# Kernel optimization log

Hardware: AMD Instinct MI355X
Metric: run time of the kernel (lower is better)

The kernel has to match this reference:

```python
import jax, jax.numpy as jnp
import numpy as np


def _lstm_last(x, wih, whh, bih, bhh):
    """PyTorch-semantics LSTM over x [B, T, I]; returns last hidden state [B, H].
    Gate order in weights: i, f, g, o (PyTorch convention)."""
    B = x.shape[0]
    H = whh.shape[1]
    b = bih + bhh

    def step(carry, xt):
        h, c = carry
        g = xt @ wih.T + h @ whh.T + b  # [B, 4H]
        i, f, gg, o = jnp.split(g, 4, axis=-1)
        c = jax.nn.sigmoid(f) * c + jax.nn.sigmoid(i) * jnp.tanh(gg)
        h = jax.nn.sigmoid(o) * jnp.tanh(c)
        return (h, c), None

    h0 = jnp.zeros((B, H), x.dtype)
    (h, _), _ = jax.lax.scan(step, (h0, h0), jnp.swapaxes(x, 0, 1))
    return h


def setup_inputs() -> dict:
    key = jax.random.key(0)
    ks = jax.random.split(key, 16)
    B, N, T = 512, 32, 50
    s = 0.05
    return {
        "agent_traj": jax.random.normal(ks[0], (B, T, 2), jnp.float32),
        "neighbour_traj": jax.random.normal(ks[1], (B, N, T, 2), jnp.float32),
        "a_wih": jax.random.normal(ks[2], (256, 2), jnp.float32) * s,
        "a_whh": jax.random.normal(ks[3], (256, 64), jnp.float32) * s,
        "a_bih": jax.random.normal(ks[4], (256,), jnp.float32) * s,
        "a_bhh": jax.random.normal(ks[5], (256,), jnp.float32) * s,
        "n_wih": jax.random.normal(ks[6], (256, 2), jnp.float32) * s,
        "n_whh": jax.random.normal(ks[7], (256, 64), jnp.float32) * s,
        "n_bih": jax.random.normal(ks[8], (256,), jnp.float32) * s,
        "n_bhh": jax.random.normal(ks[9], (256,), jnp.float32) * s,
        "d_wih": jax.random.normal(ks[10], (512, 128), jnp.float32) * s,
        "d_whh": jax.random.normal(ks[11], (512, 128), jnp.float32) * s,
        "d_bih": jax.random.normal(ks[12], (512,), jnp.float32) * s,
        "d_bhh": jax.random.normal(ks[13], (512,), jnp.float32) * s,
        "e_w": jax.random.normal(ks[14], (2, 128), jnp.float32) * s,
        "e_b": jax.random.normal(ks[15], (2,), jnp.float32) * s,
    }


def reference(agent_traj, neighbour_traj, a_wih, a_whh, a_bih, a_bhh,
              n_wih, n_whh, n_bih, n_bhh, d_wih, d_whh, d_bih, d_bhh, e_w, e_b):
    B, N, T, _ = neighbour_traj.shape
    # agent encoder: last hidden state [B, 64]
    agent_emb = _lstm_last(agent_traj, a_wih, a_whh, a_bih, a_bhh)
    # neighbour encoder: batch all B*N ragged sequences as one LSTM call, then mean over neighbours
    nh = _lstm_last(neighbour_traj.reshape(B * N, T, 2), n_wih, n_whh, n_bih, n_bhh)
    neigh_emb = nh.reshape(B, N, 64).mean(axis=1)  # [B, 64]

    h0 = jnp.concatenate([agent_emb, neigh_emb], axis=1)  # [B, 128]
    c0 = jnp.zeros_like(h0)
    db = d_bih + d_bhh

    def dec_step(carry, _):
        h, c = carry
        # LSTMCell with input = h itself
        g = h @ d_wih.T + h @ d_whh.T + db  # [B, 512]
        i, f, gg, o = jnp.split(g, 4, axis=-1)
        c = jax.nn.sigmoid(f) * c + jax.nn.sigmoid(i) * jnp.tanh(gg)
        h = jax.nn.sigmoid(o) * jnp.tanh(c)
        pred = h @ e_w.T + e_b  # [B, 2]
        return (h, c), pred

    _, preds = jax.lax.scan(dec_step, (h0, c0), None, length=30)  # [30, B, 2]
    return jnp.swapaxes(preds, 0, 1)  # [B, 30, 2]
```

## Files before the change

kernel.cpp:

```cpp
#include <hip/hip_runtime.h>
#include <hip/hip_bf16.h>


typedef __attribute__((ext_vector_type(8))) short bf16x8;
typedef __attribute__((ext_vector_type(4))) float f32x4;
typedef unsigned int uint;
typedef unsigned short ushort_t;

#define LOG2E  1.4426950408889634f
#define LOG2E2 2.8853900817779268f

__device__ __forceinline__ float rcp_fast(float x) { return __builtin_amdgcn_rcpf(x); }
__device__ __forceinline__ float exp2_fast(float x) { return __builtin_amdgcn_exp2f(x); }
__device__ __forceinline__ float sigf(float x) { return rcp_fast(1.0f + __expf(-x)); }
__device__ __forceinline__ float tanh_fast(float x) {
    x = fminf(fmaxf(x, -15.0f), 15.0f);
    float e = __expf(2.0f * x);
    return (e - 1.0f) * rcp_fast(e + 1.0f);
}
__device__ __forceinline__ ushort_t bf_hi(float f) {
    union { float f; uint u; } v; v.f = f;
    return (ushort_t)(v.u >> 16);
}
__device__ __forceinline__ ushort_t bf_rtn(float f) {
    union { float f; uint u; } v; v.f = f;
    return (ushort_t)((v.u + 0x7FFFu + ((v.u >> 16) & 1u)) >> 16);
}
__device__ __forceinline__ float bf_f(ushort_t h) {
    union { float f; uint u; } v; v.u = ((uint)h) << 16;
    return v.f;
}

__device__ __forceinline__ float cell_update_p(float xi, float xf, float xg,
                                               float xo, float& c) {
    float pi = exp2_fast(-xi);
    float pf = exp2_fast(-xf);
    float po = exp2_fast(-xo);
    float pg = exp2_fast(fminf(xg, 120.0f));
    float A = 1.0f + pf;
    float B = 1.0f + pi;
    float C = 1.0f + pg;
    float BC = B * C;
    float R  = rcp_fast(A * BC);
    float num = __builtin_fmaf(c, BC, (C - 2.0f) * A);
    float cc = num * R;
    c = cc;
    float e2 = exp2_fast(fminf(cc * LOG2E2, 120.0f));
    return (e2 - 1.0f) * rcp_fast((1.0f + po) * (e2 + 1.0f));
}

#define HS 36

__global__ __launch_bounds__(256, 4) void enc14_kernel(
    const float* __restrict__ ax, const float* __restrict__ nx,
    const float* __restrict__ a_wih, const float* __restrict__ a_whh,
    const float* __restrict__ a_bih, const float* __restrict__ a_bhh,
    const float* __restrict__ n_wih, const float* __restrict__ n_whh,
    const float* __restrict__ n_bih, const float* __restrict__ n_bhh,
    float* __restrict__ nh_out, float* __restrict__ ah_out)
{
    const int tid = threadIdx.x, blk = blockIdx.x;
    const bool agent = (blk >= 1024);
    const int seq0 = (agent ? (blk - 1024) : blk) * 16;
    const float* __restrict__ x   = agent ? ax : nx;
    const float* __restrict__ wih = agent ? a_wih : n_wih;
    const float* __restrict__ whh = agent ? a_whh : n_whh;
    const float* __restrict__ bih = agent ? a_bih : n_bih;
    const float* __restrict__ bhh = agent ? a_bhh : n_bhh;
    float* __restrict__ hout = agent ? ah_out : nh_out;

    const int lane = tid & 63, wv = tid >> 6;
    const int col = lane & 15, quad = lane >> 4;

    __shared__ __attribute__((aligned(16))) uint hb[2][16][HS];
    __shared__ __attribute__((aligned(16))) ushort_t xb[50][16][8];

    bf16x8 Aw[4][2];
    #pragma unroll
    for (int g = 0; g < 4; ++g) {
        const float sc = (g == 2) ? LOG2E2 : LOG2E;
        #pragma unroll
        for (int kt = 0; kt < 2; ++kt) {
            const float* p = whh + (size_t)(g * 64 + 16 * wv + col) * 64 + kt * 32 + quad * 8;
            float4 v0 = *(const float4*)p;
            float4 v1 = *(const float4*)(p + 4);
            float vv[8] = { v0.x, v0.y, v0.z, v0.w, v1.x, v1.y, v1.z, v1.w };
            bf16x8 h8;
            #pragma unroll
            for (int j = 0; j < 8; ++j) h8[j] = (short)bf_rtn(vv[j] * sc);
            Aw[g][kt] = h8;
        }
    }

    bf16x8 Ax[4];
    #pragma unroll
    for (int g = 0; g < 4; ++g) {
        const float sc = (g == 2) ? LOG2E2 : LOG2E;
        bf16x8 a;
        #pragma unroll
        for (int j = 0; j < 8; ++j) a[j] = 0;
        if (quad == 0) {
            const int row = g * 64 + 16 * wv + col;
            float w0 = wih[2 * row] * sc, w1 = wih[2 * row + 1] * sc;
            float b  = (bih[row] + bhh[row]) * sc;
            ushort_t w0h = bf_hi(w0), w1h = bf_hi(w1);
            ushort_t bh  = bf_hi(b);
            a[0] = (short)w0h;
            a[1] = (short)w1h;
            a[2] = (short)bf_hi(w0 - bf_f(w0h));
            a[3] = (short)bf_hi(w1 - bf_f(w1h));
            a[4] = (short)w0h;
            a[5] = (short)w1h;
            a[6] = (short)bh;
            a[7] = (short)bf_hi(b - bf_f(bh));
        }
        Ax[g] = a;
    }

    for (int idx = tid; idx < 50 * 16; idx += 256) {
        const int t = idx >> 4, s = idx & 15;
        const float* xp = x + (size_t)(seq0 + s) * 100 + 2 * t;
        float x0 = xp[0], x1 = xp[1];
        ushort_t h0 = bf_hi(x0), h1 = bf_hi(x1);
        ushort_t* e = &xb[t][s][0];
        e[0] = h0; e[1] = h1;
        e[2] = h0; e[3] = h1;
        e[4] = bf_hi(x0 - bf_f(h0));
        e[5] = bf_hi(x1 - bf_f(h1));
        e[6] = 0x3F80; e[7] = 0x3F80;
    }
    for (int i = tid; i < 16 * HS; i += 256) (&hb[0][0][0])[i] = 0u;
    __syncthreads();

    float c[4] = {0.f, 0.f, 0.f, 0.f};
    float hv[4];
    bf16x8 Bx = *(const bf16x8*)&xb[0][col][0];

    for (int t = 0; t < 50; ++t) {
        const int cur = t & 1, nxt = cur ^ 1;

        const f32x4 z4 = {0.f, 0.f, 0.f, 0.f};
        f32x4 acc[4];
        #pragma unroll
        for (int g = 0; g < 4; ++g)
            acc[g] = __builtin_amdgcn_mfma_f32_16x16x32_bf16(Ax[g], Bx, z4, 0, 0, 0);

        #pragma unroll
        for (int kt = 0; kt < 2; ++kt) {
            bf16x8 Bhi = *(const bf16x8*)&hb[cur][col][kt * 16 + quad * 4];
            #pragma unroll
            for (int g = 0; g < 4; ++g)
                acc[g] = __builtin_amdgcn_mfma_f32_16x16x32_bf16(Aw[g][kt], Bhi, acc[g], 0, 0, 0);
        }

        #pragma unroll
        for (int r = 0; r < 4; ++r)
            hv[r] = cell_update_p(acc[0][r], acc[1][r], acc[2][r], acc[3][r], c[r]);

        {
            __hip_bfloat162 p01 = __float22bfloat162_rn(make_float2(hv[0], hv[1]));
            __hip_bfloat162 p23 = __float22bfloat162_rn(make_float2(hv[2], hv[3]));
            uint2 hi2;
            union { __hip_bfloat162 b; uint u; } c0, c1;
            c0.b = p01; c1.b = p23;
            hi2.x = c0.u;
            hi2.y = c1.u;
            const int di = 8 * wv + 2 * quad;
            *(uint2*)&hb[nxt][col][di] = hi2;
        }
        if (t < 49) Bx = *(const bf16x8*)&xb[t + 1][col][0];
        __syncthreads();
    }

    {
        float4 o4 = make_float4(hv[0], hv[1], hv[2], hv[3]);
        *(float4*)(hout + (size_t)(seq0 + col) * 64 + 16 * wv + 4 * quad) = o4;
    }
}

__global__ __launch_bounds__(512) void dec14_kernel(
    const float* __restrict__ ah, const float* __restrict__ nh,
    const float* __restrict__ d_wih, const float* __restrict__ d_whh,
    const float* __restrict__ d_bih, const float* __restrict__ d_bhh,
    const float* __restrict__ e_w, const float* __restrict__ e_b,
    float* __restrict__ out)
{
    const int tid = threadIdx.x;
    const int blk = blockIdx.x;

    const int u  = tid >> 2;
    const int tt = tid & 3;
    const int r  = tt * 128 + u;

    float w[128];
    #pragma unroll
    for (int k = 0; k < 128; k += 4) {
        float4 aa = *(const float4*)(d_wih + r * 128 + k);
        float4 bb = *(const float4*)(d_whh + r * 128 + k);
        w[k]   = aa.x + bb.x;
        w[k+1] = aa.y + bb.y;
        w[k+2] = aa.z + bb.z;
        w[k+3] = aa.w + bb.w;
    }
    const float bias = d_bih[r] + d_bhh[r];

    __shared__ float hs[2][128];
    __shared__ float cs[2][128];
    __shared__ float gs[2][512];
    __shared__ float ews[2][128];
    __shared__ float ebs[2];

    if (tid < 256) {
        const int s = tid >> 7, j = tid & 127;
        const int gseq = blk * 2 + s;
        float v;
        if (j < 64) {
            v = ah[(size_t)gseq * 64 + j];
        } else {
            float acc = 0.0f;
            for (int n = 0; n < 32; ++n)
                acc += nh[(size_t)(gseq * 32 + n) * 64 + (j - 64)];
            v = acc * (1.0f / 32.0f);
        }
        hs[s][j] = v;
        cs[s][j] = 0.0f;
        ews[s][j] = e_w[tid];
    }
    if (tid < 2) ebs[tid] = e_b[tid];
    __syncthreads();

    for (int t = 0; t < 30; ++t) {
        #pragma unroll
        for (int s = 0; s < 2; ++s) {
            const float4* hp = (const float4*)(&hs[s][0]);
            float a0 = 0.f, a1 = 0.f, a2 = 0.f, a3 = 0.f;
            #pragma unroll
            for (int k = 0; k < 32; ++k) {
                float4 h4 = hp[k];
                a0 = __builtin_fmaf(w[4*k+0], h4.x, a0);
                a1 = __builtin_fmaf(w[4*k+1], h4.y, a1);
                a2 = __builtin_fmaf(w[4*k+2], h4.z, a2);
                a3 = __builtin_fmaf(w[4*k+3], h4.w, a3);
            }
            gs[s][tid] = bias + ((a0 + a1) + (a2 + a3));
        }
        __syncthreads();
        if (tid < 256) {
            const int s = tid >> 7, j = tid & 127;
            float4 g4 = *(const float4*)(&gs[s][4 * j]);
            float ig = sigf(g4.x), fg = sigf(g4.y);
            float gg = tanh_fast(g4.z), og = sigf(g4.w);
            float cc = fg * cs[s][j] + ig * gg;
            cs[s][j] = cc;
            hs[s][j] = og * tanh_fast(cc);
        }
        __syncthreads();
        {
            const int wv = tid >> 6, l = tid & 63;
            if (wv < 4) {
                const int s = wv >> 1, o = wv & 1;
                float p = hs[s][l] * ews[o][l] + hs[s][64 + l] * ews[o][64 + l];
                #pragma unroll
                for (int off = 32; off > 0; off >>= 1) p += __shfl_down(p, off);
                if (l == 0) out[((size_t)(blk * 2 + s) * 30 + t) * 2 + o] = p + ebs[o];
            }
        }
    }
}

extern "C" void kernel_launch(void* const* d_in, const int* in_sizes, int n_in,
                              void* d_out, int out_size, void* d_ws, size_t ws_size,
                              hipStream_t stream)
{
    const float* agent_traj = (const float*)d_in[0];
    const float* neigh_traj = (const float*)d_in[1];
    const float* a_wih = (const float*)d_in[2];
    const float* a_whh = (const float*)d_in[3];
    const float* a_bih = (const float*)d_in[4];
    const float* a_bhh = (const float*)d_in[5];
    const float* n_wih = (const float*)d_in[6];
    const float* n_whh = (const float*)d_in[7];
    const float* n_bih = (const float*)d_in[8];
    const float* n_bhh = (const float*)d_in[9];
    const float* d_wih = (const float*)d_in[10];
    const float* d_whh = (const float*)d_in[11];
    const float* d_bih = (const float*)d_in[12];
    const float* d_bhh = (const float*)d_in[13];
    const float* e_w   = (const float*)d_in[14];
    const float* e_b   = (const float*)d_in[15];
    float* out = (float*)d_out;

    float* nh_ws = (float*)d_ws;
    float* ah_ws = nh_ws + 16384 * 64;

    enc14_kernel<<<dim3(1024 + 32), dim3(256), 0, stream>>>(
        agent_traj, neigh_traj,
        a_wih, a_whh, a_bih, a_bhh,
        n_wih, n_whh, n_bih, n_bhh,
        nh_ws, ah_ws);

    dec14_kernel<<<dim3(256), dim3(512), 0, stream>>>(
        ah_ws, nh_ws, d_wih, d_whh, d_bih, d_bhh, e_w, e_b, out);
}
```

Before: 245.0 us.

## Process two 16-sequence tiles per encoder block to amortize weights and barriers

Each encoder block now handles 32 sequences instead of 16, running two independent MFMA chains and cell updates per wave while sharing the register-resident weight fragments. This halves the grid (528 blocks) and the number of per-timestep barriers per sequence, and gives the scheduler two independent dependency chains to interleave. The cost is higher register pressure (launch bounds relaxed to 2 blocks per CU), larger LDS usage, and fewer blocks, which may lower occupancy on a 256-CU device.

```diff
diff --git a/kernel.cpp b/kernel.cpp
--- a/kernel.cpp
+++ b/kernel.cpp
@@ -51,7 +51,7 @@
 
 #define HS 36
 
-__global__ __launch_bounds__(256, 4) void enc14_kernel(
+__global__ __launch_bounds__(256, 2) void enc17_kernel(
     const float* __restrict__ ax, const float* __restrict__ nx,
     const float* __restrict__ a_wih, const float* __restrict__ a_whh,
     const float* __restrict__ a_bih, const float* __restrict__ a_bhh,
@@ -60,8 +60,8 @@
     float* __restrict__ nh_out, float* __restrict__ ah_out)
 {
     const int tid = threadIdx.x, blk = blockIdx.x;
-    const bool agent = (blk >= 1024);
-    const int seq0 = (agent ? (blk - 1024) : blk) * 16;
+    const bool agent = (blk >= 512);
+    const int seq0 = (agent ? (blk - 512) : blk) * 32;
     const float* __restrict__ x   = agent ? ax : nx;
     const float* __restrict__ wih = agent ? a_wih : n_wih;
     const float* __restrict__ whh = agent ? a_whh : n_whh;
@@ -72,8 +72,8 @@
     const int lane = tid & 63, wv = tid >> 6;
     const int col = lane & 15, quad = lane >> 4;
 
-    __shared__ __attribute__((aligned(16))) uint hb[2][16][HS];
-    __shared__ __attribute__((aligned(16))) ushort_t xb[50][16][8];
+    __shared__ __attribute__((aligned(16))) uint hb[2][32][HS];
+    __shared__ __attribute__((aligned(16))) ushort_t xb[50][32][8];
 
     bf16x8 Aw[4][2];
     #pragma unroll
@@ -117,8 +117,8 @@
         Ax[g] = a;
     }
 
-    for (int idx = tid; idx < 50 * 16; idx += 256) {
-        const int t = idx >> 4, s = idx & 15;
+    for (int idx = tid; idx < 50 * 32; idx += 256) {
+        const int t = idx >> 5, s = idx & 31;
         const float* xp = x + (size_t)(seq0 + s) * 100 + 2 * t;
         float x0 = xp[0], x1 = xp[1];
         ushort_t h0 = bf_hi(x0), h1 = bf_hi(x1);
@@ -129,56 +129,73 @@
         e[5] = bf_hi(x1 - bf_f(h1));
         e[6] = 0x3F80; e[7] = 0x3F80;
     }
-    for (int i = tid; i < 16 * HS; i += 256) (&hb[0][0][0])[i] = 0u;
+    for (int i = tid; i < 32 * HS; i += 256) (&hb[0][0][0])[i] = 0u;
     __syncthreads();
 
-    float c[4] = {0.f, 0.f, 0.f, 0.f};
-    float hv[4];
-    bf16x8 Bx = *(const bf16x8*)&xb[0][col][0];
+    float c0[4] = {0.f, 0.f, 0.f, 0.f};
+    float c1[4] = {0.f, 0.f, 0.f, 0.f};
+    float hv0[4], hv1[4];
+    bf16x8 Bx0 = *(const bf16x8*)&xb[0][col][0];
+    bf16x8 Bx1 = *(const bf16x8*)&xb[0][col + 16][0];
 
     for (int t = 0; t < 50; ++t) {
         const int cur = t & 1, nxt = cur ^ 1;
 
         const f32x4 z4 = {0.f, 0.f, 0.f, 0.f};
-        f32x4 acc[4];
-        #pragma unroll
-        for (int g = 0; g < 4; ++g)
-            acc[g] = __builtin_amdgcn_mfma_f32_16x16x32_bf16(Ax[g], Bx, z4, 0, 0, 0);
+        f32x4 accA[4], accB[4];
+        #pragma unroll
+        for (int g = 0; g < 4; ++g) {
+            accA[g] = __builtin_amdgcn_mfma_f32_16x16x32_bf16(Ax[g], Bx0, z4, 0, 0, 0);
+            accB[g] = __builtin_amdgcn_mfma_f32_16x16x32_bf16(Ax[g], Bx1, z4, 0, 0, 0);
+        }
 
         #pragma unroll
         for (int kt = 0; kt < 2; ++kt) {
-            bf16x8 Bhi = *(const bf16x8*)&hb[cur][col][kt * 16 + quad * 4];
+            bf16x8 Bh0 = *(const bf16x8*)&hb[cur][col][kt * 16 + quad * 4];
+            bf16x8 Bh1 = *(const bf16x8*)&hb[cur][col + 16][kt * 16 + quad * 4];
             #pragma unroll
-            for (int g = 0; g < 4; ++g)
-                acc[g] = __builtin_amdgcn_mfma_f32_16x16x32_bf16(Aw[g][kt], Bhi, acc[g], 0, 0, 0);
+            for (int g = 0; g < 4; ++g) {
+                accA[g] = __builtin_amdgcn_mfma_f32_16x16x32_bf16(Aw[g][kt], Bh0, accA[g], 0, 0, 0);
+                accB[g] = __builtin_amdgcn_mfma_f32_16x16x32_bf16(Aw[g][kt], Bh1, accB[g], 0, 0, 0);
+            }
         }
 
         #pragma unroll
         for (int r = 0; r < 4; ++r)
-            hv[r] = cell_update_p(acc[0][r], acc[1][r], acc[2][r], acc[3][r], c[r]);
+            hv0[r] = cell_update_p(accA[0][r], accA[1][r], accA[2][r], accA[3][r], c0[r]);
+        #pragma unroll
+        for (int r = 0; r < 4; ++r)
+            hv1[r] = cell_update_p(accB[0][r], accB[1][r], accB[2][r], accB[3][r], c1[r]);
 
         {
-            __hip_bfloat162 p01 = __float22bfloat162_rn(make_float2(hv[0], hv[1]));
-            __hip_bfloat162 p23 = __float22bfloat162_rn(make_float2(hv[2], hv[3]));
+            union { __hip_bfloat162 b; uint u; } q0, q1;
             uint2 hi2;
-            union { __hip_bfloat162 b; uint u; } c0, c1;
-            c0.b = p01; c1.b = p23;
-            hi2.x = c0.u;
-            hi2.y = c1.u;
             const int di = 8 * wv + 2 * quad;
+            q0.b = __float22bfloat162_rn(make_float2(hv0[0], hv0[1]));
+            q1.b = __float22bfloat162_rn(make_float2(hv0[2], hv0[3]));
+            hi2.x = q0.u; hi2.y = q1.u;
             *(uint2*)&hb[nxt][col][di] = hi2;
-        }
-        if (t < 49) Bx = *(const bf16x8*)&xb[t + 1][col][0];
+            q0.b = __float22bfloat162_rn(make_float2(hv1[0], hv1[1]));
+            q1.b = __float22bfloat162_rn(make_float2(hv1[2], hv1[3]));
+            hi2.x = q0.u; hi2.y = q1.u;
+            *(uint2*)&hb[nxt][col + 16][di] = hi2;
+        }
+        if (t < 49) {
+            Bx0 = *(const bf16x8*)&xb[t + 1][col][0];
+            Bx1 = *(const bf16x8*)&xb[t + 1][col + 16][0];
+        }
         __syncthreads();
     }
 
     {
-        float4 o4 = make_float4(hv[0], hv[1], hv[2], hv[3]);
+        float4 o4 = make_float4(hv0[0], hv0[1], hv0[2], hv0[3]);
         *(float4*)(hout + (size_t)(seq0 + col) * 64 + 16 * wv + 4 * quad) = o4;
-    }
-}
-
-__global__ __launch_bounds__(512) void dec14_kernel(
+        o4 = make_float4(hv1[0], hv1[1], hv1[2], hv1[3]);
+        *(float4*)(hout + (size_t)(seq0 + 16 + col) * 64 + 16 * wv + 4 * quad) = o4;
+    }
+}
+
+__global__ __launch_bounds__(512) void dec17_kernel(
     const float* __restrict__ ah, const float* __restrict__ nh,
     const float* __restrict__ d_wih, const float* __restrict__ d_whh,
     const float* __restrict__ d_bih, const float* __restrict__ d_bhh,
@@ -293,12 +310,12 @@
     float* nh_ws = (float*)d_ws;
     float* ah_ws = nh_ws + 16384 * 64;
 
-    enc14_kernel<<<dim3(1024 + 32), dim3(256), 0, stream>>>(
+    enc17_kernel<<<dim3(512 + 16), dim3(256), 0, stream>>>(
         agent_traj, neigh_traj,
         a_wih, a_whh, a_bih, a_bhh,
         n_wih, n_whh, n_bih, n_bhh,
         nh_ws, ah_ws);
 
-    dec14_kernel<<<dim3(256), dim3(512), 0, stream>>>(
+    dec17_kernel<<<dim3(256), dim3(512), 0, stream>>>(
         ah_ws, nh_ws, d_wih, d_whh, d_bih, d_bhh, e_w, e_b, out);
 }
```

Result: slower. 258.4 us (+5.4%).
